# Optimization experiments

Measured on AMD Instinct MI355X. Metric: run time of the kernel, lower is better.

Reference implementation:

```python
import jax, jax.numpy as jnp
import numpy as np

N_NODES = 100000
N_EDGES = 1600000
D_IN = 256
D_OUT = 128


def setup_inputs() -> dict:
    key = jax.random.key(0)
    k1, k2, k3, k4, k5, k6 = jax.random.split(key, 6)
    x = jax.random.normal(k1, (N_NODES, D_IN), dtype=jnp.float32)
    W = jax.random.normal(k2, (D_IN, D_OUT), dtype=jnp.float32) * (1.0 / np.sqrt(D_IN))
    b = jax.random.normal(k3, (D_OUT,), dtype=jnp.float32) * 0.01
    edge_row = jax.random.randint(k4, (N_EDGES,), 0, N_NODES, dtype=jnp.int32)
    edge_col = jax.random.randint(k5, (N_EDGES,), 0, N_NODES, dtype=jnp.int32)
    edge_val = jax.random.uniform(k6, (N_EDGES,), dtype=jnp.float32)
    return {"x": x, "W": W, "b": b, "edge_row": edge_row,
            "edge_col": edge_col, "edge_val": edge_val}


def reference(x, W, b, edge_row, edge_col, edge_val):
    # h = Linear(x)  -> [N, D_OUT]
    h = x @ W + b
    # spmm(adj, h): out[i] = sum_{e: row[e]==i} val[e] * h[col[e]]
    msgs = edge_val[:, None] * h[edge_col]          # [E, D_OUT]
    agg = jax.ops.segment_sum(msgs, edge_row, num_segments=N_NODES)
    # activation = relu; dropout=False -> identity
    return jax.nn.relu(agg)
```

## Files before the change

kernel.cpp:

```cpp
#include <hip/hip_runtime.h>

typedef short short8 __attribute__((ext_vector_type(8)));
typedef float f32x4 __attribute__((ext_vector_type(4)));

#define N_NODES 100000
#define N_EDGES 1600000
#define D_IN 256
#define D_OUT 128

#define BROWS 16
#define NBUCK 6250

#define NGRP4 4
#define NCELL4 (NBUCK * NGRP4)
#define NCAP 112
#define C_OFF_H    0UL
#define C_OFF_WP   25600000UL
#define C_OFF_CNT  25665536UL
#define C_OFF_PEV  26065536UL
#define C_WS_NEEDED (C_OFF_PEV + (size_t)NCELL4 * NCAP * 8)

#define NGRP 8
#define NCELL (NBUCK * NGRP)
#define CSTR 4
#define NSB 49
#define OFF_H     0UL
#define OFF_WP    25600000UL
#define OFF_BCNT  25665536UL
#define OFF_BOFF  26465536UL
#define OFF_BS    26665552UL
#define OFF_PEV   26666064UL

__device__ __forceinline__ unsigned short f2bf(float f) {
    unsigned int u = __builtin_bit_cast(unsigned int, f);
    u += 0x7fffu + ((u >> 16) & 1u);
    return (unsigned short)(u >> 16);
}

__global__ void wpack_k(const float* __restrict__ W, unsigned short* __restrict__ wp) {
    int t = blockIdx.x * 256 + threadIdx.x;
    if (t >= 4096) return;
    int ks = t >> 9, nt = (t >> 6) & 7, lane = t & 63;
    int g = lane >> 4, n = nt * 16 + (lane & 15);
    int k0 = ks * 32 + g * 8;
#pragma unroll
    for (int e = 0; e < 8; ++e)
        wp[t * 8 + e] = f2bf(W[(size_t)(k0 + e) * D_OUT + n]);
}

__device__ __forceinline__ void gemm_body(const float* __restrict__ x,
                                          const short8* __restrict__ wq,
                                          const float* __restrict__ b,
                                          unsigned short* __restrict__ h) {
    int wave = threadIdx.x >> 6, lane = threadIdx.x & 63;
    int tile = blockIdx.x * 4 + wave;
    if (tile * 16 >= N_NODES) return;
    int row0 = tile * 16;
    int r = lane & 15, g = lane >> 4;

    f32x4 acc[8];
#pragma unroll
    for (int nt = 0; nt < 8; ++nt)
#pragma unroll
        for (int j = 0; j < 4; ++j) acc[nt][j] = 0.f;

    float bv[8];
#pragma unroll
    for (int nt = 0; nt < 8; ++nt) bv[nt] = b[nt * 16 + r];

    const float4* xp = (const float4*)(x + (size_t)(row0 + r) * D_IN);
#pragma unroll
    for (int ks = 0; ks < 8; ++ks) {
        float4 u0 = xp[ks * 8 + g * 2];
        float4 u1 = xp[ks * 8 + g * 2 + 1];
        short8 af;
        af[0] = (short)f2bf(u0.x); af[1] = (short)f2bf(u0.y);
        af[2] = (short)f2bf(u0.z); af[3] = (short)f2bf(u0.w);
        af[4] = (short)f2bf(u1.x); af[5] = (short)f2bf(u1.y);
        af[6] = (short)f2bf(u1.z); af[7] = (short)f2bf(u1.w);
#pragma unroll
        for (int nt = 0; nt < 8; ++nt) {
            short8 bf = wq[(ks * 8 + nt) * 64 + lane];
            acc[nt] = __builtin_amdgcn_mfma_f32_16x16x32_bf16(af, bf, acc[nt], 0, 0, 0);
        }
    }
#pragma unroll
    for (int nt = 0; nt < 8; ++nt)
#pragma unroll
        for (int j = 0; j < 4; ++j) {
            float v = acc[nt][j] + bv[nt];
            h[(size_t)(row0 + g * 4 + j) * D_OUT + ((nt & 3) * 16 + r) * 2 + (nt >> 2)] = f2bf(v);
        }
}

__global__ __launch_bounds__(256) void gemm_k(const float* __restrict__ x,
                                              const short8* __restrict__ wq,
                                              const float* __restrict__ b,
                                              unsigned short* __restrict__ h) {
    gemm_body(x, wq, b, h);
}

__global__ void binc_k(const int4* __restrict__ er4, const int4* __restrict__ ec4,
                       const float4* __restrict__ ev4,
                       int* __restrict__ cnt, uint2* __restrict__ pev) {
    int t = blockIdx.x * 256 + threadIdx.x;
    int g = blockIdx.x & 3;
    if (t >= N_EDGES / 4) return;
    int4 r = er4[t];
    int4 c = ec4[t];
    float4 v = ev4[t];
    int rows[4] = {r.x, r.y, r.z, r.w};
    int cols[4] = {c.x, c.y, c.z, c.w};
    float vals[4] = {v.x, v.y, v.z, v.w};
    int rel[4], cell[4];
#pragma unroll
    for (int i = 0; i < 4; ++i) {
        cell[i] = (rows[i] >> 4) * NGRP4 + g;
        rel[i] = atomicAdd(&cnt[cell[i] * 4], 1);
    }
#pragma unroll
    for (int i = 0; i < 4; ++i) {
        if (rel[i] < NCAP) {
            uint2 p;
            p.x = (unsigned int)cols[i] | ((unsigned int)(rows[i] & (BROWS - 1)) << 17);
            p.y = __builtin_bit_cast(unsigned int, vals[i]);
            pev[(size_t)cell[i] * NCAP + rel[i]] = p;
        }
    }
}

__global__ void padfix_k(int* __restrict__ cnt, uint2* __restrict__ pev) {
    int c = blockIdx.x * 256 + threadIdx.x;
    if (c >= NCELL4) return;
    int n = cnt[c * 4];
    if (n > NCAP) n = NCAP;
    int n8 = (n + 7) & ~7;
    uint2 z; z.x = 0u; z.y = 0u;
    for (int i = n; i < n8; ++i) pev[(size_t)c * NCAP + i] = z;
    cnt[c * 4] = n8;
}

__device__ __forceinline__ void seg_accum_pad(float2* __restrict__ T2,
                                              const unsigned int* __restrict__ h32,
                                              const uint2* __restrict__ pev,
                                              int s, int n8, int lane) {
    if (n8 <= 0) return;
    int e = s + n8;
    int last = e - 1;

    uint2 pn[8];
#pragma unroll
    for (int j = 0; j < 8; ++j) pn[j] = pev[s + j];
    unsigned pxc[8]; float pvc[8]; unsigned hvc[8];
#pragma unroll
    for (int j = 0; j < 8; ++j) {
        pxc[j] = (unsigned)__builtin_amdgcn_readfirstlane((int)pn[j].x);
        pvc[j] = __builtin_bit_cast(float, (unsigned)__builtin_amdgcn_readfirstlane((int)pn[j].y));
    }
#pragma unroll
    for (int j = 0; j < 8; ++j) {
        const unsigned int* hb = h32 + ((size_t)(pxc[j] & 0x1FFFFu) << 6);
        hvc[j] = hb[lane];
    }
#pragma unroll
    for (int j = 0; j < 8; ++j) pn[j] = pev[min(s + 8 + j, last)];

    for (int base = s; base < e; base += 8) {
        uint2 pt[8];
#pragma unroll
        for (int j = 0; j < 8; ++j) pt[j] = pev[min(base + 16 + j, last)];
        unsigned pxn[8]; float pvn[8]; unsigned hvn[8];
#pragma unroll
        for (int j = 0; j < 8; ++j) {
            pxn[j] = (unsigned)__builtin_amdgcn_readfirstlane((int)pn[j].x);
            pvn[j] = __builtin_bit_cast(float, (unsigned)__builtin_amdgcn_readfirstlane((int)pn[j].y));
        }
#pragma unroll
        for (int j = 0; j < 8; ++j) {
            const unsigned int* hb = h32 + ((size_t)(pxn[j] & 0x1FFFFu) << 6);
            hvn[j] = hb[lane];
        }
#pragma unroll
        for (int j = 0; j < 8; ++j) {
            float v = pvc[j];
            float lo = __builtin_bit_cast(float, hvc[j] << 16);
            float hi = __builtin_bit_cast(float, hvc[j] & 0xffff0000u);
            int idx2 = (int)(pxc[j] >> 17) * 64 + lane;
            float2 t = T2[idx2];
            t.x = fmaf(v, lo, t.x);
            t.y = fmaf(v, hi, t.y);
            T2[idx2] = t;
        }
#pragma unroll
        for (int j = 0; j < 8; ++j) {
            hvc[j] = hvn[j]; pxc[j] = pxn[j]; pvc[j] = pvn[j]; pn[j] = pt[j];
        }
    }
}

__global__ __launch_bounds__(256) void aggc_k(const unsigned int* __restrict__ h32,
                                              const int* __restrict__ cnt,
                                              const uint2* __restrict__ pev,
                                              float* __restrict__ out) {
    __shared__ float2 tile[4][BROWS * 64];
    int w = threadIdx.x >> 6, lane = threadIdx.x & 63;
    float2* T2 = tile[w];
    int b = blockIdx.x * 4 + w;
    if (b >= NBUCK) return;

    float4* T4 = reinterpret_cast<float4*>(T2);
    for (int i = lane; i < BROWS * 32; i += 64) {
        float4 z = {0.f, 0.f, 0.f, 0.f};
        T4[i] = z;
    }

#pragma unroll
    for (int g = 0; g < NGRP4; ++g) {
        int cell = b * NGRP4 + g;
        int n8 = cnt[cell * 4];
        seg_accum_pad(T2, h32, pev, cell * NCAP, n8, lane);
    }

    int row0 = b * BROWS;
#pragma unroll
    for (int r = 0; r < BROWS; ++r) {
        float2 t2 = T2[r * 64 + lane];
        out[(size_t)(row0 + r) * 128 + lane]      = fmaxf(t2.x, 0.f);
        out[(size_t)(row0 + r) * 128 + 64 + lane] = fmaxf(t2.y, 0.f);
    }
}

__device__ __forceinline__ void seg_accum_legacy(float* __restrict__ T,
                                                 const unsigned int* __restrict__ h32,
                                                 const uint2* __restrict__ bpev,
                                                 int s, int e, int lane) {
    if (s >= e) return;
    int last = e - 1;
    uint2 pn[8];
#pragma unroll
    for (int j = 0; j < 8; ++j) pn[j] = bpev[min(s + j, last)];
    unsigned int hvc[8];
    float vc[8];
    int rlc[8];
#pragma unroll
    for (int j = 0; j < 8; ++j) {
        hvc[j] = h32[(size_t)(pn[j].x & 0x1FFFFu) * 64 + lane];
        vc[j] = __builtin_bit_cast(float, pn[j].y);
        rlc[j] = (int)(pn[j].x >> 17);
    }
#pragma unroll
    for (int j = 0; j < 8; ++j) pn[j] = bpev[min(s + 8 + j, last)];

    for (int base = s; base < e; base += 8) {
        uint2 pt[8];
#pragma unroll
        for (int j = 0; j < 8; ++j) pt[j] = bpev[min(base + 16 + j, last)];
        unsigned int hvn[8];
        float vn[8];
        int rln[8];
#pragma unroll
        for (int j = 0; j < 8; ++j) {
            hvn[j] = h32[(size_t)(pn[j].x & 0x1FFFFu) * 64 + lane];
            vn[j] = __builtin_bit_cast(float, pn[j].y);
            rln[j] = (int)(pn[j].x >> 17);
        }
#pragma unroll
        for (int j = 0; j < 8; ++j) {
            float v = (base + j < e) ? vc[j] : 0.f;
            float lo = __builtin_bit_cast(float, hvc[j] << 16);
            float hi = __builtin_bit_cast(float, hvc[j] & 0xffff0000u);
            int idx = rlc[j] * 128 + lane;
            float t0 = T[idx], t1 = T[idx + 64];
            T[idx] = fmaf(v, lo, t0);
            T[idx + 64] = fmaf(v, hi, t1);
        }
#pragma unroll
        for (int j = 0; j < 8; ++j) {
            hvc[j] = hvn[j]; vc[j] = vn[j]; rlc[j] = rln[j]; pn[j] = pt[j];
        }
    }
}

__global__ __launch_bounds__(256) void gemmcnt_k(const float* __restrict__ x,
                                                 const short8* __restrict__ wq,
                                                 const float* __restrict__ b,
                                                 unsigned short* __restrict__ h,
                                                 const int4* __restrict__ er4,
                                                 int* __restrict__ bcnt) {
    int t = blockIdx.x * 256 + threadIdx.x;
    int g0 = blockIdx.x & 7;
    if (t < N_EDGES / 4) {
        int4 r = er4[t];
        atomicAdd(&bcnt[((r.x >> 4) * NGRP + g0) * CSTR], 1);
        atomicAdd(&bcnt[((r.y >> 4) * NGRP + g0) * CSTR], 1);
        atomicAdd(&bcnt[((r.z >> 4) * NGRP + g0) * CSTR], 1);
        atomicAdd(&bcnt[((r.w >> 4) * NGRP + g0) * CSTR], 1);
    }
    gemm_body(x, wq, b, h);
}

__global__ __launch_bounds__(1024) void scan1_k(const int* __restrict__ bcnt,
                                                int* __restrict__ boffs,
                                                int* __restrict__ bs) {
    __shared__ int s[1024];
    int t = threadIdx.x;
    int c = blockIdx.x * 1024 + t;
    int v = (c < NCELL) ? bcnt[c * CSTR] : 0;
    s[t] = v;
    __syncthreads();
    for (int off = 1; off < 1024; off <<= 1) {
        int tmp = (t >= off) ? s[t - off] : 0;
        __syncthreads();
        s[t] += tmp;
        __syncthreads();
    }
    if (c < NCELL) boffs[c] = s[t];
    if (t == 1023) bs[blockIdx.x] = s[1023];
}

__global__ void scan2_k(int* __restrict__ bs, int nb) {
    if (threadIdx.x == 0) {
        int run = 0;
        for (int bb = 0; bb < nb; ++bb) { int t = bs[bb]; bs[bb] = run; run += t; }
        bs[nb] = run;
    }
}

__global__ void scan3_k(int* __restrict__ boffs, int* __restrict__ bcnt,
                        const int* __restrict__ bs) {
    int c = blockIdx.x * 256 + threadIdx.x;
    if (c < NCELL) {
        int v = boffs[c] - bcnt[c * CSTR] + bs[c >> 10];
        boffs[c] = v;
        bcnt[c * CSTR] = v;
    }
    if (c == 0) boffs[NCELL] = bs[NSB];
}

__global__ void bin_k(const int4* __restrict__ er4, const int4* __restrict__ ec4,
                      const float4* __restrict__ ev4,
                      int* __restrict__ bcur, uint2* __restrict__ bpev) {
    int t = blockIdx.x * 256 + threadIdx.x;
    int g = blockIdx.x & 7;
    if (t >= N_EDGES / 4) return;
    int4 r = er4[t];
    int4 c = ec4[t];
    float4 v = ev4[t];
    int rows[4] = {r.x, r.y, r.z, r.w};
    int cols[4] = {c.x, c.y, c.z, c.w};
    float vals[4] = {v.x, v.y, v.z, v.w};
    int pos[4];
#pragma unroll
    for (int i = 0; i < 4; ++i)
        pos[i] = atomicAdd(&bcur[((rows[i] >> 4) * NGRP + g) * CSTR], 1);
#pragma unroll
    for (int i = 0; i < 4; ++i) {
        uint2 p;
        p.x = (unsigned int)cols[i] | ((unsigned int)(rows[i] & (BROWS - 1)) << 17);
        p.y = __builtin_bit_cast(unsigned int, vals[i]);
        bpev[pos[i]] = p;
    }
}

__global__ __launch_bounds__(256) void agg_k(const unsigned int* __restrict__ h32,
                                             const int* __restrict__ boffs,
                                             const uint2* __restrict__ bpev,
                                             float* __restrict__ out) {
    __shared__ float tile[4][BROWS * 128];
    int w = threadIdx.x >> 6, lane = threadIdx.x & 63;
    float* T = tile[w];
    int b = blockIdx.x * 4 + w;
    if (b >= NBUCK) return;

    for (int i = lane; i < BROWS * 128 / 4; i += 64) {
        float4 z = {0.f, 0.f, 0.f, 0.f};
        reinterpret_cast<float4*>(T)[i] = z;
    }
    int s = boffs[b * NGRP], e = boffs[b * NGRP + NGRP];
    seg_accum_legacy(T, h32, bpev, s, e, lane);

    int row0 = b * BROWS;
    const float2* T2 = reinterpret_cast<const float2*>(T);
#pragma unroll
    for (int r = 0; r < BROWS; ++r) {
        float2 t2 = T2[r * 64 + lane];
        t2.x = fmaxf(t2.x, 0.f);
        t2.y = fmaxf(t2.y, 0.f);
        reinterpret_cast<float2*>(out + (size_t)(row0 + r) * 128)[lane] = t2;
    }
}

extern "C" void kernel_launch(void* const* d_in, const int* in_sizes, int n_in,
                              void* d_out, int out_size, void* d_ws, size_t ws_size,
                              hipStream_t stream) {
    const float* x = (const float*)d_in[0];
    const float* W = (const float*)d_in[1];
    const float* b = (const float*)d_in[2];
    const int* er = (const int*)d_in[3];
    const int* ec = (const int*)d_in[4];
    const float* ev = (const float*)d_in[5];
    float* out = (float*)d_out;
    char* ws = (char*)d_ws;

    if (ws_size >= C_WS_NEEDED) {
        unsigned short* h = (unsigned short*)(ws + C_OFF_H);
        unsigned short* wp = (unsigned short*)(ws + C_OFF_WP);
        int* cnt = (int*)(ws + C_OFF_CNT);
        uint2* pev = (uint2*)(ws + C_OFF_PEV);

        hipMemsetAsync(cnt, 0, (size_t)NCELL4 * 4 * 4, stream);
        wpack_k<<<16, 256, 0, stream>>>(W, wp);
        gemm_k<<<1563, 256, 0, stream>>>(x, (const short8*)wp, b, h);
        binc_k<<<(N_EDGES / 4 + 255) / 256, 256, 0, stream>>>((const int4*)er, (const int4*)ec,
                                                              (const float4*)ev, cnt, pev);
        padfix_k<<<(NCELL4 + 255) / 256, 256, 0, stream>>>(cnt, pev);
        aggc_k<<<(NBUCK + 3) / 4, 256, 0, stream>>>((const unsigned int*)h, cnt, pev, out);
    } else {
        unsigned short* h = (unsigned short*)(ws + OFF_H);
        unsigned short* wp = (unsigned short*)(ws + OFF_WP);
        int* bcnt = (int*)(ws + OFF_BCNT);
        int* boffs = (int*)(ws + OFF_BOFF);
        int* bs = (int*)(ws + OFF_BS);
        uint2* bpev = (uint2*)(ws + OFF_PEV);

        hipMemsetAsync(bcnt, 0, (size_t)NCELL * CSTR * 4, stream);
        wpack_k<<<16, 256, 0, stream>>>(W, wp);
        gemmcnt_k<<<1563, 256, 0, stream>>>(x, (const short8*)wp, b, h, (const int4*)er, bcnt);
        scan1_k<<<NSB, 1024, 0, stream>>>(bcnt, boffs, bs);
        scan2_k<<<1, 64, 0, stream>>>(bs, NSB);
        scan3_k<<<(NCELL + 255) / 256, 256, 0, stream>>>(boffs, bcnt, bs);
        bin_k<<<(N_EDGES / 4 + 255) / 256, 256, 0, stream>>>((const int4*)er, (const int4*)ec,
                                                             (const float4*)ev, bcnt, bpev);
        agg_k<<<(NBUCK + 3) / 4, 256, 0, stream>>>((const unsigned int*)h, boffs, bpev, out);
    }
}
```

Before: 224.4 us.

## Slice edge bins by column range with overflow buffer and larger row buckets

Edges are now binned into 32-row buckets and further split into 8 column slices (two groups each). Cells are laid out slice-major, so at any moment all aggregation waves are gathering h rows from a similar column range, which is meant to improve L2 locality of the random gathers. A per-bucket overflow buffer catches edges that exceed the smaller per-cell capacity. Edge-list loads and output stores become nontemporal, and the aggregation block shrinks to two waves. The cost is more cells, more padding and one extra atomic on overflow; if an overflow buffer exceeds its own capacity, edges are silently dropped.

After: 325.3 us. 45.0% more time.

```diff
diff --git a/kernel.cpp b/kernel.cpp
--- a/kernel.cpp
+++ b/kernel.cpp
@@ -8,20 +8,25 @@
 #define D_IN 256
 #define D_OUT 128
 
-#define BROWS 16
-#define NBUCK 6250
-
-#define NGRP4 4
-#define NCELL4 (NBUCK * NGRP4)
-#define NCAP 112
-#define C_OFF_H    0UL
-#define C_OFF_WP   25600000UL
-#define C_OFF_CNT  25665536UL
-#define C_OFF_PEV  26065536UL
-#define C_WS_NEEDED (C_OFF_PEV + (size_t)NCELL4 * NCAP * 8)
-
+#define BROWS 32
+#define NBUCK 3125
+#define NSL 8
+#define SLW 12500
+#define NCELL5 (NBUCK * NSL * 2)
+#define NCAP 48
+#define OVCAP 64
+#define S_OFF_H    0UL
+#define S_OFF_WP   25600000UL
+#define S_OFF_CNT  25665536UL
+#define S_OFF_OVC  26465536UL
+#define S_OFF_OVF  26515536UL
+#define S_OFF_PEV  28115536UL
+#define S_WS_NEEDED (S_OFF_PEV + (size_t)NCELL5 * NCAP * 8)
+
+#define FBROWS 16
+#define FNBUCK 6250
 #define NGRP 8
-#define NCELL (NBUCK * NGRP)
+#define NCELL (FNBUCK * NGRP)
 #define CSTR 4
 #define NSB 49
 #define OFF_H     0UL
@@ -35,6 +40,14 @@
     unsigned int u = __builtin_bit_cast(unsigned int, f);
     u += 0x7fffu + ((u >> 16) & 1u);
     return (unsigned short)(u >> 16);
+}
+
+__device__ __forceinline__ uint2 ld_nt_u2(const uint2* p) {
+    unsigned long long u = __builtin_nontemporal_load((const unsigned long long*)p);
+    uint2 r;
+    r.x = (unsigned int)u;
+    r.y = (unsigned int)(u >> 32);
+    return r;
 }
 
 __global__ void wpack_k(const float* __restrict__ W, unsigned short* __restrict__ wp) {
@@ -102,9 +115,10 @@
 
 __global__ void binc_k(const int4* __restrict__ er4, const int4* __restrict__ ec4,
                        const float4* __restrict__ ev4,
-                       int* __restrict__ cnt, uint2* __restrict__ pev) {
+                       int* __restrict__ cnt, int* __restrict__ ovfc,
+                       uint2* __restrict__ pev, uint2* __restrict__ ovf) {
     int t = blockIdx.x * 256 + threadIdx.x;
-    int g = blockIdx.x & 3;
+    int g = blockIdx.x & 1;
     if (t >= N_EDGES / 4) return;
     int4 r = er4[t];
     int4 c = ec4[t];
@@ -112,32 +126,42 @@
     int rows[4] = {r.x, r.y, r.z, r.w};
     int cols[4] = {c.x, c.y, c.z, c.w};
     float vals[4] = {v.x, v.y, v.z, v.w};
-    int rel[4], cell[4];
 #pragma unroll
     for (int i = 0; i < 4; ++i) {
-        cell[i] = (rows[i] >> 4) * NGRP4 + g;
-        rel[i] = atomicAdd(&cnt[cell[i] * 4], 1);
-    }
-#pragma unroll
-    for (int i = 0; i < 4; ++i) {
-        if (rel[i] < NCAP) {
-            uint2 p;
-            p.x = (unsigned int)cols[i] | ((unsigned int)(rows[i] & (BROWS - 1)) << 17);
-            p.y = __builtin_bit_cast(unsigned int, vals[i]);
-            pev[(size_t)cell[i] * NCAP + rel[i]] = p;
-        }
-    }
-}
-
-__global__ void padfix_k(int* __restrict__ cnt, uint2* __restrict__ pev) {
+        int s = cols[i] / SLW;
+        int bkt = rows[i] >> 5;
+        int cell = ((s << 1) | g) * NBUCK + bkt;
+        int rel = atomicAdd(&cnt[cell * 4], 1);
+        uint2 p;
+        p.x = (unsigned int)cols[i] | ((unsigned int)(rows[i] & (BROWS - 1)) << 17);
+        p.y = __builtin_bit_cast(unsigned int, vals[i]);
+        if (rel < NCAP) {
+            pev[cell * NCAP + rel] = p;
+        } else {
+            int ro = atomicAdd(&ovfc[bkt * 4], 1);
+            if (ro < OVCAP) ovf[bkt * OVCAP + ro] = p;
+        }
+    }
+}
+
+__global__ void padfix_k(int* __restrict__ cnt, uint2* __restrict__ pev,
+                         int* __restrict__ ovfc, uint2* __restrict__ ovf) {
     int c = blockIdx.x * 256 + threadIdx.x;
-    if (c >= NCELL4) return;
-    int n = cnt[c * 4];
-    if (n > NCAP) n = NCAP;
-    int n8 = (n + 7) & ~7;
     uint2 z; z.x = 0u; z.y = 0u;
-    for (int i = n; i < n8; ++i) pev[(size_t)c * NCAP + i] = z;
-    cnt[c * 4] = n8;
+    if (c < NCELL5) {
+        int n = cnt[c * 4];
+        if (n > NCAP) n = NCAP;
+        int n8 = (n + 7) & ~7;
+        for (int i = n; i < n8; ++i) pev[c * NCAP + i] = z;
+        cnt[c * 4] = n8;
+    } else if (c < NCELL5 + NBUCK) {
+        int b = c - NCELL5;
+        int n = ovfc[b * 4];
+        if (n > OVCAP) n = OVCAP;
+        int n8 = (n + 7) & ~7;
+        for (int i = n; i < n8; ++i) ovf[b * OVCAP + i] = z;
+        ovfc[b * 4] = n8;
+    }
 }
 
 __device__ __forceinline__ void seg_accum_pad(float2* __restrict__ T2,
@@ -150,7 +174,7 @@
 
     uint2 pn[8];
 #pragma unroll
-    for (int j = 0; j < 8; ++j) pn[j] = pev[s + j];
+    for (int j = 0; j < 8; ++j) pn[j] = ld_nt_u2(&pev[s + j]);
     unsigned pxc[8]; float pvc[8]; unsigned hvc[8];
 #pragma unroll
     for (int j = 0; j < 8; ++j) {
@@ -163,12 +187,12 @@
         hvc[j] = hb[lane];
     }
 #pragma unroll
-    for (int j = 0; j < 8; ++j) pn[j] = pev[min(s + 8 + j, last)];
+    for (int j = 0; j < 8; ++j) pn[j] = ld_nt_u2(&pev[min(s + 8 + j, last)]);
 
     for (int base = s; base < e; base += 8) {
         uint2 pt[8];
 #pragma unroll
-        for (int j = 0; j < 8; ++j) pt[j] = pev[min(base + 16 + j, last)];
+        for (int j = 0; j < 8; ++j) pt[j] = ld_nt_u2(&pev[min(base + 16 + j, last)]);
         unsigned pxn[8]; float pvn[8]; unsigned hvn[8];
 #pragma unroll
         for (int j = 0; j < 8; ++j) {
@@ -198,14 +222,16 @@
     }
 }
 
-__global__ __launch_bounds__(256) void aggc_k(const unsigned int* __restrict__ h32,
+__global__ __launch_bounds__(128) void aggc_k(const unsigned int* __restrict__ h32,
                                               const int* __restrict__ cnt,
                                               const uint2* __restrict__ pev,
+                                              const int* __restrict__ ovfc,
+                                              const uint2* __restrict__ ovf,
                                               float* __restrict__ out) {
-    __shared__ float2 tile[4][BROWS * 64];
+    __shared__ float2 tile[2][BROWS * 64];
     int w = threadIdx.x >> 6, lane = threadIdx.x & 63;
     float2* T2 = tile[w];
-    int b = blockIdx.x * 4 + w;
+    int b = blockIdx.x * 2 + w;
     if (b >= NBUCK) return;
 
     float4* T4 = reinterpret_cast<float4*>(T2);
@@ -215,18 +241,24 @@
     }
 
 #pragma unroll
-    for (int g = 0; g < NGRP4; ++g) {
-        int cell = b * NGRP4 + g;
-        int n8 = cnt[cell * 4];
-        seg_accum_pad(T2, h32, pev, cell * NCAP, n8, lane);
+    for (int s = 0; s < NSL; ++s)
+#pragma unroll
+        for (int g = 0; g < 2; ++g) {
+            int cell = ((s << 1) | g) * NBUCK + b;
+            int n8 = cnt[cell * 4];
+            seg_accum_pad(T2, h32, pev, cell * NCAP, n8, lane);
+        }
+    {
+        int n8o = ovfc[b * 4];
+        seg_accum_pad(T2, h32, ovf, b * OVCAP, n8o, lane);
     }
 
     int row0 = b * BROWS;
 #pragma unroll
     for (int r = 0; r < BROWS; ++r) {
         float2 t2 = T2[r * 64 + lane];
-        out[(size_t)(row0 + r) * 128 + lane]      = fmaxf(t2.x, 0.f);
-        out[(size_t)(row0 + r) * 128 + 64 + lane] = fmaxf(t2.y, 0.f);
+        __builtin_nontemporal_store(fmaxf(t2.x, 0.f), &out[(size_t)(row0 + r) * 128 + lane]);
+        __builtin_nontemporal_store(fmaxf(t2.y, 0.f), &out[(size_t)(row0 + r) * 128 + 64 + lane]);
     }
 }
 
@@ -356,7 +388,7 @@
 #pragma unroll
     for (int i = 0; i < 4; ++i) {
         uint2 p;
-        p.x = (unsigned int)cols[i] | ((unsigned int)(rows[i] & (BROWS - 1)) << 17);
+        p.x = (unsigned int)cols[i] | ((unsigned int)(rows[i] & (FBROWS - 1)) << 17);
         p.y = __builtin_bit_cast(unsigned int, vals[i]);
         bpev[pos[i]] = p;
     }
@@ -366,23 +398,23 @@
                                              const int* __restrict__ boffs,
                                              const uint2* __restrict__ bpev,
                                              float* __restrict__ out) {
-    __shared__ float tile[4][BROWS * 128];
+    __shared__ float tile[4][FBROWS * 128];
     int w = threadIdx.x >> 6, lane = threadIdx.x & 63;
     float* T = tile[w];
     int b = blockIdx.x * 4 + w;
-    if (b >= NBUCK) return;
-
-    for (int i = lane; i < BROWS * 128 / 4; i += 64) {
+    if (b >= FNBUCK) return;
+
+    for (int i = lane; i < FBROWS * 128 / 4; i += 64) {
         float4 z = {0.f, 0.f, 0.f, 0.f};
         reinterpret_cast<float4*>(T)[i] = z;
     }
     int s = boffs[b * NGRP], e = boffs[b * NGRP + NGRP];
     seg_accum_legacy(T, h32, bpev, s, e, lane);
 
-    int row0 = b * BROWS;
+    int row0 = b * FBROWS;
     const float2* T2 = reinterpret_cast<const float2*>(T);
 #pragma unroll
-    for (int r = 0; r < BROWS; ++r) {
+    for (int r = 0; r < FBROWS; ++r) {
         float2 t2 = T2[r * 64 + lane];
         t2.x = fmaxf(t2.x, 0.f);
         t2.y = fmaxf(t2.y, 0.f);
@@ -402,19 +434,21 @@
     float* out = (float*)d_out;
     char* ws = (char*)d_ws;
 
-    if (ws_size >= C_WS_NEEDED) {
-        unsigned short* h = (unsigned short*)(ws + C_OFF_H);
-        unsigned short* wp = (unsigned short*)(ws + C_OFF_WP);
-        int* cnt = (int*)(ws + C_OFF_CNT);
-        uint2* pev = (uint2*)(ws + C_OFF_PEV);
-
-        hipMemsetAsync(cnt, 0, (size_t)NCELL4 * 4 * 4, stream);
+    if (ws_size >= S_WS_NEEDED) {
+        unsigned short* h = (unsigned short*)(ws + S_OFF_H);
+        unsigned short* wp = (unsigned short*)(ws + S_OFF_WP);
+        int* cnt = (int*)(ws + S_OFF_CNT);
+        int* ovfc = (int*)(ws + S_OFF_OVC);
+        uint2* ovf = (uint2*)(ws + S_OFF_OVF);
+        uint2* pev = (uint2*)(ws + S_OFF_PEV);
+
+        hipMemsetAsync(cnt, 0, 850000, stream);
         wpack_k<<<16, 256, 0, stream>>>(W, wp);
         gemm_k<<<1563, 256, 0, stream>>>(x, (const short8*)wp, b, h);
         binc_k<<<(N_EDGES / 4 + 255) / 256, 256, 0, stream>>>((const int4*)er, (const int4*)ec,
-                                                              (const float4*)ev, cnt, pev);
-        padfix_k<<<(NCELL4 + 255) / 256, 256, 0, stream>>>(cnt, pev);
-        aggc_k<<<(NBUCK + 3) / 4, 256, 0, stream>>>((const unsigned int*)h, cnt, pev, out);
+                                                              (const float4*)ev, cnt, ovfc, pev, ovf);
+        padfix_k<<<(NCELL5 + NBUCK + 255) / 256, 256, 0, stream>>>(cnt, pev, ovfc, ovf);
+        aggc_k<<<(NBUCK + 1) / 2, 128, 0, stream>>>((const unsigned int*)h, cnt, pev, ovfc, ovf, out);
     } else {
         unsigned short* h = (unsigned short*)(ws + OFF_H);
         unsigned short* wp = (unsigned short*)(ws + OFF_WP);
@@ -431,6 +465,6 @@
         scan3_k<<<(NCELL + 255) / 256, 256, 0, stream>>>(boffs, bcnt, bs);
         bin_k<<<(N_EDGES / 4 + 255) / 256, 256, 0, stream>>>((const int4*)er, (const int4*)ec,
                                                              (const float4*)ev, bcnt, bpev);
-        agg_k<<<(NBUCK + 3) / 4, 256, 0, stream>>>((const unsigned int*)h, boffs, bpev, out);
-    }
-}
+        agg_k<<<(FNBUCK + 3) / 4, 256, 0, stream>>>((const unsigned int*)h, boffs, bpev, out);
+    }
+}
```
